# Kernel optimization log

Hardware: AMD Instinct MI355X
Metric: run time of the kernel (lower is better)

Reference implementation:

```python
import jax, jax.numpy as jnp
import numpy as np

B, L1, LQ, LA, H = 32, 512, 32, 32, 128  # dialog turns, doc len, q len, a len, hidden
NEG = -1e30  # finite stand-in for torch's -inf (avoids NaN for fully-masked row 0, which is dropped by zero_first anyway)


def setup_inputs() -> dict:
    key = jax.random.key(0)
    ks = jax.random.split(key, 6)
    return {
        "xd_emb": jax.random.normal(ks[0], (B, L1, H), jnp.float32),
        "xq_emb": jax.random.normal(ks[1], (B, LQ, H), jnp.float32),
        "xa_emb": jax.random.normal(ks[2], (B, LA, H), jnp.float32),
        "W": jax.random.normal(ks[3], (H, H), jnp.float32) / np.sqrt(H).astype(np.float32),
        "b": jnp.zeros((H,), jnp.float32),
        "recency_weight": jnp.full((1,), -0.5, jnp.float32),
        "xq_mask": jax.random.randint(ks[4], (B, LQ), 0, 2).astype(bool),
        "xa_mask": jax.random.randint(ks[5], (B, LA), 0, 2).astype(bool),
    }


def _forward(xd_emb, xq_emb, xa_emb, W, b, recency_weight, xq_mask, xa_mask):
    Bn = xq_emb.shape[0]
    M = xq_emb.shape[1] + xa_emb.shape[1]  # max_dialog_len (max_qa_len)
    dlg = jnp.concatenate([xq_emb, xa_emb], axis=1).reshape(Bn * M, -1)  # (B*M, h) flattened dialog
    pad_mask = jnp.concatenate([xq_mask, xa_mask], axis=1).reshape(-1)    # (B*M,)

    ts = jnp.arange(Bn)
    j_ts = jnp.arange(Bn * M) // M  # timestep of each flattened dialog token
    # triu(ones, k=0) repeated M times along cols: timestep i masks tokens of timesteps >= i
    causal = j_ts[None, :] >= ts[:, None]            # (B, B*M)
    y_mask = causal | pad_mask[None, :]              # (B, B*M), True = masked

    # Linear + ReLU projections; y_proj computed once (no explicit (B, B*M, h) tiling)
    x_proj = jax.nn.relu(xd_emb @ W.T + b)           # (B, L1, h)
    y_proj = jax.nn.relu(dlg @ W.T + b)              # (B*M, h)

    scores = jnp.einsum('bld,kd->blk', x_proj, y_proj)      # (B, L1, B*M)
    scores = jnp.where(y_mask[:, None, :], jnp.float32(NEG), scores)

    # toeplitz recency bias: |i - j_ts| * recency_weight, row 0 zeroed (zero_first)
    rw = recency_weight[0] * jnp.abs(ts[:, None] - j_ts[None, :]).astype(jnp.float32)
    rw = jnp.concatenate([jnp.zeros_like(rw[:1]), rw[1:]], axis=0)
    scores = scores + rw[:, None, :]

    alpha = jax.nn.softmax(scores, axis=-1)
    alpha = jnp.concatenate([jnp.zeros_like(alpha[:1]), alpha[1:]], axis=0)  # zero_first
    return jnp.einsum('blk,kd->bld', alpha, dlg)     # weighted sum over original (unprojected) dialog


def reference(xd_emb, xq_emb, xa_emb, W, b, recency_weight, xq_mask, xa_mask):
    return _forward(xd_emb, xq_emb, xa_emb, W, b, recency_weight, xq_mask, xa_mask)
```

## Files before the change

kernel.cpp:

```cpp
#include <hip/hip_runtime.h>
#include <stdint.h>

#define NEGV (-1e30f)

constexpr int L1_ = 512;
constexpr int H_  = 128;
constexpr int NK_ = 2048;

typedef __attribute__((ext_vector_type(8))) _Float16 f16x8;
typedef __attribute__((ext_vector_type(2))) __fp16   h16x2;
typedef __attribute__((ext_vector_type(4))) float    f32x4;

static __device__ __forceinline__ uint16_t f2h(float x) {
    union { _Float16 h; uint16_t u; } cv; cv.h = (_Float16)x; return cv.u;
}


__global__ __launch_bounds__(256) void preproc_kernel(
        const float* __restrict__ xq,
        const float* __restrict__ xa,
        const float* __restrict__ W,
        const float* __restrict__ bias,
        const uint8_t* __restrict__ qm,
        const uint8_t* __restrict__ am,
        uint8_t* __restrict__ Y2,
        uint8_t* __restrict__ V2,
        uint8_t* __restrict__ W2,
        float* __restrict__ badd) {
    int b = blockIdx.x;
    int tid = threadIdx.x;
    __shared__ __align__(16) float sbuf[64 * 128];

    if (b < 128) {
        int k0 = b * 16;
        f32x4* xr4 = (f32x4*)sbuf;
#pragma unroll
        for (int i = 0; i < 2; ++i) {
            int idx = tid + i * 256;
            int row = idx >> 5, d4 = idx & 31;
            int k = k0 + row;
            int b2 = k >> 6, r = k & 63;
            const float* src = (r < 32) ? (xq + (size_t)(b2 * 32 + r) * H_)
                                        : (xa + (size_t)(b2 * 32 + (r - 32)) * H_);
            xr4[idx] = *(const f32x4*)(src + d4 * 4);
        }
        __syncthreads();
        int c = tid & 127, rh = tid >> 7;
        float acc[8];
#pragma unroll
        for (int i = 0; i < 8; ++i) acc[i] = 0.0f;
        const f32x4* w4 = (const f32x4*)(W + (size_t)c * H_);
        for (int d4 = 0; d4 < 32; ++d4) {
            f32x4 wv = w4[d4];
#pragma unroll
            for (int i = 0; i < 8; ++i) {
                f32x4 x = xr4[(rh * 8 + i) * 32 + d4];
                acc[i] += wv[0]*x[0] + wv[1]*x[1] + wv[2]*x[2] + wv[3]*x[3];
            }
        }
        float bc = bias[c];
        float* res = sbuf + 2048;
#pragma unroll
        for (int i = 0; i < 8; ++i)
            res[(rh * 8 + i) * H_ + c] = fmaxf(acc[i] + bc, 0.0f);
        __syncthreads();
        int ks = tid >> 6, l = tid & 63, n16 = l & 15, g = l >> 4;
        uint16_t hbuf[8];
#pragma unroll
        for (int j = 0; j < 8; ++j)
            hbuf[j] = f2h(res[n16 * H_ + ks * 32 + g * 8 + j]);
        uint8_t* dst = Y2 + (((size_t)b * 4 + ks) << 10) + l * 16;
        *(uint64_t*)dst       = ((const uint64_t*)hbuf)[0];
        *(uint64_t*)(dst + 8) = ((const uint64_t*)hbuf)[1];
    } else if (b < 160) {
        int kt = b - 128;
        f32x4* ld4 = (f32x4*)sbuf;
#pragma unroll
        for (int i = 0; i < 8; ++i) {
            int idx = tid + i * 256;
            int row = idx >> 5, d4 = idx & 31;
            const float* src = (row < 32) ? (xq + (size_t)(kt * 32 + row) * H_)
                                          : (xa + (size_t)(kt * 32 + row - 32) * H_);
            ld4[idx] = *(const f32x4*)(src + d4 * 4);
        }
        __syncthreads();
#pragma unroll
        for (int i = 0; i < 4; ++i) {
            int id = tid + i * 256;
            int cT = id >> 7, ks = (id >> 6) & 1, l = id & 63;
            int n16 = l & 15, g = l >> 4;
            uint16_t hbuf[8];
#pragma unroll
            for (int j = 0; j < 8; ++j)
                hbuf[j] = f2h(sbuf[(ks * 32 + g * 8 + j) * H_ + cT * 16 + n16]);
            uint8_t* dst = V2 + (((size_t)kt * 16 + cT * 2 + ks) << 10) + l * 16;
            *(uint64_t*)dst       = ((const uint64_t*)hbuf)[0];
            *(uint64_t*)(dst + 8) = ((const uint64_t*)hbuf)[1];
        }
    } else if (b == 160) {
        int* flags = (int*)sbuf;
        if (tid == 0) { flags[0] = 0; flags[1] = 0; }
        __syncthreads();
        uint32_t v = ((const uint32_t*)qm)[tid] | ((const uint32_t*)am)[tid];
        if (v & 0xFFu)        atomicOr(&flags[0], 1);
        if (v & 0xFFFFFF00u)  atomicOr(&flags[1], 1);
        __syncthreads();
        int f0 = flags[0], f1 = flags[1];
        int mode = (f0 && !f1) ? 0 : ((!f0 && f1) ? 1 : 2);
        for (int k = tid; k < NK_; k += 256) {
            int b2 = k >> 6, r = k & 63;
            int idx = b2 * 32 + (r < 32 ? r : r - 32);
            const uint8_t* src = (r < 32) ? qm : am;
            int p;
            if (mode == 0)      p = (((const int*)src)[idx] != 0);
            else if (mode == 1) p = (((const float*)src)[idx] != 0.0f);
            else                p = (src[idx] != 0);
            badd[k] = p ? NEGV : 0.0f;
        }
    } else {
        for (int h = 0; h < 2; ++h) {
            f32x4* s4 = (f32x4*)sbuf;
#pragma unroll
            for (int i = 0; i < 8; ++i) {
                int idx = tid + i * 256;
                s4[idx] = *(const f32x4*)(W + (size_t)h * 64 * H_ + idx * 4);
            }
            __syncthreads();
#pragma unroll
            for (int i = 0; i < 4; ++i) {
                int id = tid + i * 256;
                int ct = id >> 8, ks = (id >> 6) & 3, l = id & 63;
                int n16 = l & 15, g = l >> 4;
                uint16_t hb[8];
#pragma unroll
                for (int j = 0; j < 8; ++j)
                    hb[j] = f2h(sbuf[(ct * 16 + n16) * H_ + ks * 32 + g * 8 + j]);
                uint8_t* dst = W2 + (((size_t)((h * 4 + ct) * 4 + ks)) << 10) + l * 16;
                *(uint64_t*)dst       = ((const uint64_t*)hb)[0];
                *(uint64_t*)(dst + 8) = ((const uint64_t*)hb)[1];
            }
            __syncthreads();
        }
    }
}

__global__ __launch_bounds__(512, 2) void attn_kernel(
        const float*   __restrict__ xd,
        const uint8_t* __restrict__ W2,
        const float*   __restrict__ bias,
        const uint8_t* __restrict__ Y2,
        const uint8_t* __restrict__ V2,
        const float*   __restrict__ badd,
        const float*   __restrict__ rw,
        float* __restrict__ out) {
    int bid = blockIdx.x;
    int t, lt;
    if (bid < 256) { int p = bid >> 4; t = (p < 15) ? 31 - p : 16; lt = bid & 15; }
    else           { int b2 = bid - 256; int p = b2 >> 4; t = (p < 15) ? p + 1 : 0; lt = b2 & 15; }
    int l0 = lt << 5;
    int tid = threadIdx.x;

    __shared__ __align__(16) float smem[16384];
    __shared__ float stats_m[8][32];
    __shared__ float stats_l[8][32];

    if (t == 0) {
        f32x4 z = {0.f, 0.f, 0.f, 0.f};
        f32x4* o4 = (f32x4*)(out + (size_t)l0 * H_);
        for (int i = tid; i < 32 * H_ / 4; i += 512) o4[i] = z;
        return;
    }

    int w = tid >> 6, lane = tid & 63, n16 = lane & 15, g = lane >> 4;
    int prow0 = n16, prow1 = 16 + n16;
    int swzP = (n16 & 7) << 4;

    uint16_t* xbuf  = (uint16_t*)((char*)smem + 32768);
    uint16_t* xpbuf = (uint16_t*)((char*)smem + 40960);
    {
        const float* xsrc = xd + (size_t)(t * L1_ + l0) * H_;
#pragma unroll
        for (int i = 0; i < 2; ++i) {
            int idx = tid + i * 512;
            int row = idx >> 5, c4 = idx & 31;
            f32x4 v = *(const f32x4*)(xsrc + idx * 4);
            uint16_t hb[4] = { f2h(v[0]), f2h(v[1]), f2h(v[2]), f2h(v[3]) };
            *(uint64_t*)((char*)xbuf + row * 256 + ((c4 * 8) ^ ((row & 7) << 4)))
                = *(const uint64_t*)hb;
        }
    }
    __syncthreads();
    {
        f16x8 af[2][4];
#pragma unroll
        for (int rT = 0; rT < 2; ++rT) {
            int row = rT * 16 + n16, swz = (row & 7) << 4;
#pragma unroll
            for (int ks = 0; ks < 4; ++ks)
                af[rT][ks] = *(const f16x8*)((char*)xbuf + row * 256 + ((ks * 64 + g * 16) ^ swz));
        }
        f32x4 z4 = {0.f, 0.f, 0.f, 0.f};
        f32x4 d0 = z4, d1 = z4;
#pragma unroll
        for (int ks = 0; ks < 4; ++ks) {
            f16x8 wf = *(const f16x8*)(W2 + (((size_t)w * 4 + ks) << 10) + lane * 16);
            d0 = __builtin_amdgcn_mfma_f32_16x16x32_f16(af[0][ks], wf, d0, 0, 0, 0);
            d1 = __builtin_amdgcn_mfma_f32_16x16x32_f16(af[1][ks], wf, d1, 0, 0, 0);
        }
        float bb = bias[w * 16 + n16];
#pragma unroll
        for (int rT = 0; rT < 2; ++rT) {
            const f32x4& d = rT ? d1 : d0;
#pragma unroll
            for (int q = 0; q < 4; ++q) {
                int row = rT * 16 + g * 4 + q, swz = (row & 7) << 4;
                *(uint16_t*)((char*)xpbuf + row * 256 + (((w * 16 + n16) * 2) ^ swz))
                    = f2h(fmaxf(d[q] + bb, 0.0f));
            }
        }
    }
    __syncthreads();
    f16x8 xf[2][4];
#pragma unroll
    for (int rT = 0; rT < 2; ++rT) {
        int row = rT * 16 + n16, swz = (row & 7) << 4;
#pragma unroll
        for (int ks = 0; ks < 4; ++ks)
            xf[rT][ks] = *(const f16x8*)((char*)xpbuf + row * 256 + ((ks * 64 + g * 16) ^ swz));
    }

    f32x4 zero4 = {0.f, 0.f, 0.f, 0.f};
    f32x4 acc[2][8];
#pragma unroll
    for (int a = 0; a < 2; ++a)
#pragma unroll
        for (int c = 0; c < 8; ++c) acc[a][c] = zero4;

    float m_r[2] = {-INFINITY, -INFINITY};
    float l_r[2] = {0.0f, 0.0f};
    float rww = rw[0];

    char* Pw = (char*)smem + w * 4096;

    for (int kt = w; kt < t; kt += 8) {
        const uint8_t* ybase = Y2 + ((size_t)kt << 14) + lane * 16;
        const uint8_t* vbase = V2 + ((size_t)kt << 14) + lane * 16;

        f16x8 yf[4][4];
#pragma unroll
        for (int kkT = 0; kkT < 4; ++kkT)
#pragma unroll
            for (int ks = 0; ks < 4; ++ks)
                yf[kkT][ks] = *(const f16x8*)(ybase + ((kkT * 4 + ks) << 10));
        f16x8 vbA[4][2];
#pragma unroll
        for (int cT = 0; cT < 4; ++cT) {
            vbA[cT][0] = *(const f16x8*)(vbase + ((cT * 2) << 10));
            vbA[cT][1] = *(const f16x8*)(vbase + ((cT * 2 + 1) << 10));
        }
        f32x4 ba4[4];
#pragma unroll
        for (int kkT = 0; kkT < 4; ++kkT)
            ba4[kkT] = *(const f32x4*)(badd + kt * 64 + kkT * 16 + g * 4);

        f32x4 ss[4][2];
#pragma unroll
        for (int kkT = 0; kkT < 4; ++kkT) { ss[kkT][0] = zero4; ss[kkT][1] = zero4; }
        __builtin_amdgcn_s_setprio(1);
#pragma unroll
        for (int ks = 0; ks < 4; ++ks)
#pragma unroll
            for (int kkT = 0; kkT < 4; ++kkT) {
                ss[kkT][0] = __builtin_amdgcn_mfma_f32_16x16x32_f16(yf[kkT][ks], xf[0][ks], ss[kkT][0], 0, 0, 0);
                ss[kkT][1] = __builtin_amdgcn_mfma_f32_16x16x32_f16(yf[kkT][ks], xf[1][ks], ss[kkT][1], 0, 0, 0);
            }
        __builtin_amdgcn_s_setprio(0);

        f16x8 vbB[4][2];
#pragma unroll
        for (int cT = 0; cT < 4; ++cT) {
            vbB[cT][0] = *(const f16x8*)(vbase + (((cT + 4) * 2) << 10));
            vbB[cT][1] = *(const f16x8*)(vbase + (((cT + 4) * 2 + 1) << 10));
        }

        float biasK = rww * (float)(t - kt);
#pragma unroll
        for (int kkT = 0; kkT < 4; ++kkT) {
            f32x4 ba = ba4[kkT] + biasK;
            ss[kkT][0] += ba;
            ss[kkT][1] += ba;
        }

        float sc[2];
#pragma unroll
        for (int rT = 0; rT < 2; ++rT) {
            f32x4 mx4 = ss[0][rT];
#pragma unroll
            for (int kkT = 1; kkT < 4; ++kkT) {
                mx4[0] = fmaxf(mx4[0], ss[kkT][rT][0]);
                mx4[1] = fmaxf(mx4[1], ss[kkT][rT][1]);
                mx4[2] = fmaxf(mx4[2], ss[kkT][rT][2]);
                mx4[3] = fmaxf(mx4[3], ss[kkT][rT][3]);
            }
            float mx = fmaxf(fmaxf(mx4[0], mx4[1]), fmaxf(mx4[2], mx4[3]));
            mx = fmaxf(mx, __shfl_xor(mx, 16));
            mx = fmaxf(mx, __shfl_xor(mx, 32));
            float mn = fmaxf(m_r[rT], mx);
            sc[rT] = __expf(m_r[rT] - mn);
            m_r[rT] = mn;
        }

#pragma unroll
        for (int rT = 0; rT < 2; ++rT) {
            int r = rT ? prow1 : prow0;
            float mn = m_r[rT];
            float ps = 0.0f;
#pragma unroll
            for (int kkT = 0; kkT < 4; ++kkT) {
                f32x4 p;
#pragma unroll
                for (int q = 0; q < 4; ++q) p[q] = __expf(ss[kkT][rT][q] - mn);
                ps += (p[0] + p[1]) + (p[2] + p[3]);
                union { h16x2 h2[2]; uint64_t u64; } pk;
                pk.h2[0] = __builtin_amdgcn_cvt_pkrtz(p[0], p[1]);
                pk.h2[1] = __builtin_amdgcn_cvt_pkrtz(p[2], p[3]);
                *(uint64_t*)(Pw + r * 128 + ((kkT * 32 + g * 8) ^ swzP)) = pk.u64;
            }
            ps += __shfl_xor(ps, 16);
            ps += __shfl_xor(ps, 32);
            l_r[rT] = l_r[rT] * sc[rT] + ps;
        }

        asm volatile("s_waitcnt lgkmcnt(0)" ::: "memory");

        if (!__all((sc[0] == 1.0f) && (sc[1] == 1.0f))) {
#pragma unroll
            for (int rT = 0; rT < 2; ++rT) {
                f32x4 s4;
#pragma unroll
                for (int q = 0; q < 4; ++q) s4[q] = __shfl(sc[rT], (g << 2) + q);
#pragma unroll
                for (int cT = 0; cT < 8; ++cT) acc[rT][cT] *= s4;
            }
        }

        f16x8 pa[2][2];
#pragma unroll
        for (int rT = 0; rT < 2; ++rT) {
            int r = rT ? prow1 : prow0;
#pragma unroll
            for (int ks = 0; ks < 2; ++ks)
                pa[rT][ks] = *(const f16x8*)(Pw + r * 128 + ((ks * 64 + g * 16) ^ swzP));
        }
        __builtin_amdgcn_s_setprio(1);
#pragma unroll
        for (int cT = 0; cT < 4; ++cT)
#pragma unroll
            for (int rT = 0; rT < 2; ++rT) {
                acc[rT][cT] = __builtin_amdgcn_mfma_f32_16x16x32_f16(pa[rT][0], vbA[cT][0], acc[rT][cT], 0, 0, 0);
                acc[rT][cT] = __builtin_amdgcn_mfma_f32_16x16x32_f16(pa[rT][1], vbA[cT][1], acc[rT][cT], 0, 0, 0);
            }
#pragma unroll
        for (int cT = 0; cT < 4; ++cT)
#pragma unroll
            for (int rT = 0; rT < 2; ++rT) {
                acc[rT][cT + 4] = __builtin_amdgcn_mfma_f32_16x16x32_f16(pa[rT][0], vbB[cT][0], acc[rT][cT + 4], 0, 0, 0);
                acc[rT][cT + 4] = __builtin_amdgcn_mfma_f32_16x16x32_f16(pa[rT][1], vbB[cT][1], acc[rT][cT + 4], 0, 0, 0);
            }
        __builtin_amdgcn_s_setprio(0);
    }

    if (g == 0) {
        stats_m[w][n16]      = m_r[0];
        stats_m[w][16 + n16] = m_r[1];
        stats_l[w][n16]      = l_r[0];
        stats_l[w][16 + n16] = l_r[1];
    }
    __syncthreads();

    float fac[2][4];
#pragma unroll
    for (int rT = 0; rT < 2; ++rT)
#pragma unroll
        for (int q = 0; q < 4; ++q) {
            int r = rT * 16 + (g << 2) + q;
            float mf = stats_m[0][r];
#pragma unroll
            for (int wv = 1; wv < 8; ++wv) mf = fmaxf(mf, stats_m[wv][r]);
            float lf = 0.0f;
#pragma unroll
            for (int wv = 0; wv < 8; ++wv) lf += stats_l[wv][r] * __expf(stats_m[wv][r] - mf);
            fac[rT][q] = __expf(stats_m[w][r] - mf) / lf;
        }

    size_t obase = (size_t)(t * L1_ + l0) * H_;
    for (int rT = 0; rT < 2; ++rT) {
        float* Ob = smem + w * 2048;
#pragma unroll
        for (int cT = 0; cT < 8; ++cT)
#pragma unroll
            for (int q = 0; q < 4; ++q)
                Ob[(cT * 4 + q) * 64 + lane] = acc[rT][cT][q] * fac[rT][q];
        __syncthreads();
#pragma unroll
        for (int s = 0; s < 4; ++s) {
            int slot = w * 4 + s;
            float v = 0.0f;
#pragma unroll
            for (int wv = 0; wv < 8; ++wv) v += smem[wv * 2048 + slot * 64 + lane];
            int cT = slot >> 2, q = slot & 3;
            out[obase + (size_t)(rT * 16 + (g << 2) + q) * H_ + cT * 16 + n16] = v;
        }
        __syncthreads();
    }
}

extern "C" void kernel_launch(void* const* d_in, const int* in_sizes, int n_in,
                              void* d_out, int out_size, void* d_ws, size_t ws_size,
                              hipStream_t stream) {
    const float*   xd   = (const float*)d_in[0];
    const float*   xq   = (const float*)d_in[1];
    const float*   xa   = (const float*)d_in[2];
    const float*   W    = (const float*)d_in[3];
    const float*   bias = (const float*)d_in[4];
    const float*   rw   = (const float*)d_in[5];
    const uint8_t* qm   = (const uint8_t*)d_in[6];
    const uint8_t* am   = (const uint8_t*)d_in[7];
    float* out = (float*)d_out;

    char* ws = (char*)d_ws;
    float*   badd = (float*)ws;
    uint8_t* Y2   = (uint8_t*)(ws + 8192);
    uint8_t* V2   = (uint8_t*)(ws + 8192 + 524288);
    uint8_t* W2   = (uint8_t*)(ws + 8192 + 2 * 524288);

    preproc_kernel<<<162, 256, 0, stream>>>(xq, xa, W, bias, qm, am,
                                            Y2, V2, W2, badd);
    attn_kernel<<<512, 512, 0, stream>>>(xd, W2, bias, Y2, V2, badd, rw, out);
}
```

Baseline: 44.74 us.

## Restructure attention kernel with LDS double-buffered K/V tiles and 64-row blocks

The attention kernel now processes 64 query rows per block, using 256 blocks instead of 512. Four row groups each take two key-timestep halves. Y and V tiles for each pair of timesteps are staged into LDS with global_load_lds, double-buffered so the next pair loads while the current one computes. Previously every wave read Y and V straight from global memory. The two half-softmax partials are merged at the end through LDS. The trade-offs are one block per CU with about 144KB of LDS, a __syncthreads per iteration, and the removal of the old load-balancing block order across timesteps.

```diff
diff --git a/kernel.cpp b/kernel.cpp
--- a/kernel.cpp
+++ b/kernel.cpp
@@ -13,6 +13,12 @@
 
 static __device__ __forceinline__ uint16_t f2h(float x) {
     union { _Float16 h; uint16_t u; } cv; cv.h = (_Float16)x; return cv.u;
+}
+
+static __device__ __forceinline__ void gload16(const void* g, void* l) {
+    __builtin_amdgcn_global_load_lds(
+        (const __attribute__((address_space(1))) uint32_t*)g,
+        (__attribute__((address_space(3))) uint32_t*)l, 16, 0, 0);
 }
 
 
@@ -144,7 +150,7 @@
     }
 }
 
-__global__ __launch_bounds__(512, 2) void attn_kernel(
+__global__ __launch_bounds__(512, 1) void attn_kernel(
         const float*   __restrict__ xd,
         const uint8_t* __restrict__ W2,
         const float*   __restrict__ bias,
@@ -154,264 +160,241 @@
         const float*   __restrict__ rw,
         float* __restrict__ out) {
     int bid = blockIdx.x;
-    int t, lt;
-    if (bid < 256) { int p = bid >> 4; t = (p < 15) ? 31 - p : 16; lt = bid & 15; }
-    else           { int b2 = bid - 256; int p = b2 >> 4; t = (p < 15) ? p + 1 : 0; lt = b2 & 15; }
-    int l0 = lt << 5;
+    int t  = bid >> 3;
+    int l0 = (bid & 7) << 6;
     int tid = threadIdx.x;
 
-    __shared__ __align__(16) float smem[16384];
-    __shared__ float stats_m[8][32];
-    __shared__ float stats_l[8][32];
+    __shared__ __align__(16) char LDSA[147456];
+    __shared__ float stats_m[8][16];
+    __shared__ float stats_l[8][16];
 
     if (t == 0) {
         f32x4 z = {0.f, 0.f, 0.f, 0.f};
         f32x4* o4 = (f32x4*)(out + (size_t)l0 * H_);
-        for (int i = tid; i < 32 * H_ / 4; i += 512) o4[i] = z;
+        for (int i = tid; i < 64 * H_ / 4; i += 512) o4[i] = z;
         return;
     }
 
     int w = tid >> 6, lane = tid & 63, n16 = lane & 15, g = lane >> 4;
-    int prow0 = n16, prow1 = 16 + n16;
-    int swzP = (n16 & 7) << 4;
-
-    uint16_t* xbuf  = (uint16_t*)((char*)smem + 32768);
-    uint16_t* xpbuf = (uint16_t*)((char*)smem + 40960);
+    int rg = w & 3, kh = w >> 2;
+    int swz = (n16 & 7) << 4;
+
+    {
+        char* ld = LDSA;
+        gload16(Y2 + tid * 16,        ld + tid * 16);
+        gload16(Y2 + tid * 16 + 8192, ld + tid * 16 + 8192);
+        gload16(V2 + tid * 16,         ld + 16384 + tid * 16);
+        gload16(V2 + tid * 16 + 8192,  ld + 24576 + tid * 16);
+        if (1 < t) {
+            const uint8_t* gy = Y2 + (1 << 14);
+            const uint8_t* gv = V2 + (1 << 14);
+            char* ld2 = LDSA + 32768;
+            gload16(gy + tid * 16,        ld2 + tid * 16);
+            gload16(gy + tid * 16 + 8192, ld2 + tid * 16 + 8192);
+            gload16(gv + tid * 16,         ld2 + 16384 + tid * 16);
+            gload16(gv + tid * 16 + 8192,  ld2 + 24576 + tid * 16);
+        }
+    }
+
+    char* xbuf  = LDSA + 65536;
+    char* xpbuf = LDSA + 131072;
     {
         const float* xsrc = xd + (size_t)(t * L1_ + l0) * H_;
 #pragma unroll
-        for (int i = 0; i < 2; ++i) {
+        for (int i = 0; i < 4; ++i) {
             int idx = tid + i * 512;
             int row = idx >> 5, c4 = idx & 31;
             f32x4 v = *(const f32x4*)(xsrc + idx * 4);
             uint16_t hb[4] = { f2h(v[0]), f2h(v[1]), f2h(v[2]), f2h(v[3]) };
-            *(uint64_t*)((char*)xbuf + row * 256 + ((c4 * 8) ^ ((row & 7) << 4)))
-                = *(const uint64_t*)hb;
+            *(uint64_t*)(xbuf + row * 256 + ((c4 * 8) ^ ((row & 7) << 4))) = *(const uint64_t*)hb;
         }
     }
     __syncthreads();
     {
-        f16x8 af[2][4];
-#pragma unroll
-        for (int rT = 0; rT < 2; ++rT) {
-            int row = rT * 16 + n16, swz = (row & 7) << 4;
-#pragma unroll
-            for (int ks = 0; ks < 4; ++ks)
-                af[rT][ks] = *(const f16x8*)((char*)xbuf + row * 256 + ((ks * 64 + g * 16) ^ swz));
-        }
+        f16x8 af[4];
+        int arow = rg * 16 + n16;
+#pragma unroll
+        for (int ks = 0; ks < 4; ++ks)
+            af[ks] = *(const f16x8*)(xbuf + arow * 256 + ((ks * 64 + g * 16) ^ swz));
         f32x4 z4 = {0.f, 0.f, 0.f, 0.f};
-        f32x4 d0 = z4, d1 = z4;
-#pragma unroll
-        for (int ks = 0; ks < 4; ++ks) {
-            f16x8 wf = *(const f16x8*)(W2 + (((size_t)w * 4 + ks) << 10) + lane * 16);
-            d0 = __builtin_amdgcn_mfma_f32_16x16x32_f16(af[0][ks], wf, d0, 0, 0, 0);
-            d1 = __builtin_amdgcn_mfma_f32_16x16x32_f16(af[1][ks], wf, d1, 0, 0, 0);
-        }
-        float bb = bias[w * 16 + n16];
-#pragma unroll
-        for (int rT = 0; rT < 2; ++rT) {
-            const f32x4& d = rT ? d1 : d0;
+        f32x4 d[4] = {z4, z4, z4, z4};
+#pragma unroll
+        for (int c = 0; c < 4; ++c)
+#pragma unroll
+            for (int ks = 0; ks < 4; ++ks) {
+                f16x8 wf = *(const f16x8*)(W2 + (((size_t)(kh * 4 + c) * 4 + ks) << 10) + lane * 16);
+                d[c] = __builtin_amdgcn_mfma_f32_16x16x32_f16(af[ks], wf, d[c], 0, 0, 0);
+            }
+#pragma unroll
+        for (int c = 0; c < 4; ++c) {
+            int col = (kh * 4 + c) * 16 + n16;
+            float bb = bias[col];
 #pragma unroll
             for (int q = 0; q < 4; ++q) {
-                int row = rT * 16 + g * 4 + q, swz = (row & 7) << 4;
-                *(uint16_t*)((char*)xpbuf + row * 256 + (((w * 16 + n16) * 2) ^ swz))
-                    = f2h(fmaxf(d[q] + bb, 0.0f));
+                int row2 = rg * 16 + g * 4 + q;
+                *(uint16_t*)(xpbuf + row2 * 256 + ((col * 2) ^ ((row2 & 7) << 4)))
+                    = f2h(fmaxf(d[c][q] + bb, 0.0f));
             }
         }
     }
     __syncthreads();
-    f16x8 xf[2][4];
-#pragma unroll
-    for (int rT = 0; rT < 2; ++rT) {
-        int row = rT * 16 + n16, swz = (row & 7) << 4;
+    f16x8 xf[4];
+    {
+        int arow = rg * 16 + n16;
 #pragma unroll
         for (int ks = 0; ks < 4; ++ks)
-            xf[rT][ks] = *(const f16x8*)((char*)xpbuf + row * 256 + ((ks * 64 + g * 16) ^ swz));
-    }
+            xf[ks] = *(const f16x8*)(xpbuf + arow * 256 + ((ks * 64 + g * 16) ^ swz));
+    }
+    __syncthreads();
 
     f32x4 zero4 = {0.f, 0.f, 0.f, 0.f};
-    f32x4 acc[2][8];
-#pragma unroll
-    for (int a = 0; a < 2; ++a)
-#pragma unroll
-        for (int c = 0; c < 8; ++c) acc[a][c] = zero4;
-
-    float m_r[2] = {-INFINITY, -INFINITY};
-    float l_r[2] = {0.0f, 0.0f};
+    f32x4 acc[8];
+#pragma unroll
+    for (int c = 0; c < 8; ++c) acc[c] = zero4;
+    float m_r = -INFINITY, l_r = 0.0f;
     float rww = rw[0];
-
-    char* Pw = (char*)smem + w * 4096;
-
-    for (int kt = w; kt < t; kt += 8) {
-        const uint8_t* ybase = Y2 + ((size_t)kt << 14) + lane * 16;
-        const uint8_t* vbase = V2 + ((size_t)kt << 14) + lane * 16;
-
-        f16x8 yf[4][4];
-#pragma unroll
-        for (int kkT = 0; kkT < 4; ++kkT)
-#pragma unroll
-            for (int ks = 0; ks < 4; ++ks)
-                yf[kkT][ks] = *(const f16x8*)(ybase + ((kkT * 4 + ks) << 10));
-        f16x8 vbA[4][2];
-#pragma unroll
-        for (int cT = 0; cT < 4; ++cT) {
-            vbA[cT][0] = *(const f16x8*)(vbase + ((cT * 2) << 10));
-            vbA[cT][1] = *(const f16x8*)(vbase + ((cT * 2 + 1) << 10));
-        }
-        f32x4 ba4[4];
-#pragma unroll
-        for (int kkT = 0; kkT < 4; ++kkT)
-            ba4[kkT] = *(const f32x4*)(badd + kt * 64 + kkT * 16 + g * 4);
-
-        f32x4 ss[4][2];
-#pragma unroll
-        for (int kkT = 0; kkT < 4; ++kkT) { ss[kkT][0] = zero4; ss[kkT][1] = zero4; }
-        __builtin_amdgcn_s_setprio(1);
-#pragma unroll
-        for (int ks = 0; ks < 4; ++ks)
+    char* Pw = LDSA + 131072 + w * 2048;
+    int nR = (t + 1) >> 1;
+
+    for (int i = 0; i < nR; ++i) {
+        int cur = i & 1;
+        if (i + 1 < nR) {
+            int kt0 = 2 * (i + 1);
+            char* ld = LDSA + (cur ? 0 : 65536);
+            const uint8_t* gy = Y2 + ((size_t)kt0 << 14);
+            const uint8_t* gv = V2 + ((size_t)kt0 << 14);
+            gload16(gy + tid * 16,        ld + tid * 16);
+            gload16(gy + tid * 16 + 8192, ld + tid * 16 + 8192);
+            gload16(gv + tid * 16,         ld + 16384 + tid * 16);
+            gload16(gv + tid * 16 + 8192,  ld + 24576 + tid * 16);
+            if (kt0 + 1 < t) {
+                gy += (1 << 14); gv += (1 << 14);
+                char* ld2 = ld + 32768;
+                gload16(gy + tid * 16,        ld2 + tid * 16);
+                gload16(gy + tid * 16 + 8192, ld2 + tid * 16 + 8192);
+                gload16(gv + tid * 16,         ld2 + 16384 + tid * 16);
+                gload16(gv + tid * 16 + 8192,  ld2 + 24576 + tid * 16);
+            }
+        }
+
+        int kt = 2 * i + kh;
+        if (kt < t) {
+            const char* Yb = LDSA + (cur ? 65536 : 0) + kh * 32768;
+            const char* Vb = Yb + 16384;
+
+            f32x4 ss[4];
+#pragma unroll
+            for (int kkT = 0; kkT < 4; ++kkT) ss[kkT] = zero4;
+            __builtin_amdgcn_s_setprio(1);
+#pragma unroll
+            for (int ks = 0; ks < 4; ++ks) {
+                f16x8 yf[4];
+#pragma unroll
+                for (int kkT = 0; kkT < 4; ++kkT)
+                    yf[kkT] = *(const f16x8*)(Yb + ((kkT * 4 + ks) << 10) + lane * 16);
+#pragma unroll
+                for (int kkT = 0; kkT < 4; ++kkT)
+                    ss[kkT] = __builtin_amdgcn_mfma_f32_16x16x32_f16(yf[kkT], xf[ks], ss[kkT], 0, 0, 0);
+            }
+            __builtin_amdgcn_s_setprio(0);
+
+            float biasK = rww * (float)(t - kt);
 #pragma unroll
             for (int kkT = 0; kkT < 4; ++kkT) {
-                ss[kkT][0] = __builtin_amdgcn_mfma_f32_16x16x32_f16(yf[kkT][ks], xf[0][ks], ss[kkT][0], 0, 0, 0);
-                ss[kkT][1] = __builtin_amdgcn_mfma_f32_16x16x32_f16(yf[kkT][ks], xf[1][ks], ss[kkT][1], 0, 0, 0);
-            }
-        __builtin_amdgcn_s_setprio(0);
-
-        f16x8 vbB[4][2];
-#pragma unroll
-        for (int cT = 0; cT < 4; ++cT) {
-            vbB[cT][0] = *(const f16x8*)(vbase + (((cT + 4) * 2) << 10));
-            vbB[cT][1] = *(const f16x8*)(vbase + (((cT + 4) * 2 + 1) << 10));
-        }
-
-        float biasK = rww * (float)(t - kt);
-#pragma unroll
-        for (int kkT = 0; kkT < 4; ++kkT) {
-            f32x4 ba = ba4[kkT] + biasK;
-            ss[kkT][0] += ba;
-            ss[kkT][1] += ba;
-        }
-
-        float sc[2];
-#pragma unroll
-        for (int rT = 0; rT < 2; ++rT) {
-            f32x4 mx4 = ss[0][rT];
+                f32x4 ba = *(const f32x4*)(badd + kt * 64 + kkT * 16 + g * 4);
+                ss[kkT] += (ba + biasK);
+            }
+
+            f32x4 mx4 = ss[0];
 #pragma unroll
             for (int kkT = 1; kkT < 4; ++kkT) {
-                mx4[0] = fmaxf(mx4[0], ss[kkT][rT][0]);
-                mx4[1] = fmaxf(mx4[1], ss[kkT][rT][1]);
-                mx4[2] = fmaxf(mx4[2], ss[kkT][rT][2]);
-                mx4[3] = fmaxf(mx4[3], ss[kkT][rT][3]);
+                mx4[0] = fmaxf(mx4[0], ss[kkT][0]);
+                mx4[1] = fmaxf(mx4[1], ss[kkT][1]);
+                mx4[2] = fmaxf(mx4[2], ss[kkT][2]);
+                mx4[3] = fmaxf(mx4[3], ss[kkT][3]);
             }
             float mx = fmaxf(fmaxf(mx4[0], mx4[1]), fmaxf(mx4[2], mx4[3]));
             mx = fmaxf(mx, __shfl_xor(mx, 16));
             mx = fmaxf(mx, __shfl_xor(mx, 32));
-            float mn = fmaxf(m_r[rT], mx);
-            sc[rT] = __expf(m_r[rT] - mn);
-            m_r[rT] = mn;
-        }
-
-#pragma unroll
-        for (int rT = 0; rT < 2; ++rT) {
-            int r = rT ? prow1 : prow0;
-            float mn = m_r[rT];
+            float mn = fmaxf(m_r, mx);
+            float sc = __expf(m_r - mn);
+            m_r = mn;
+
             float ps = 0.0f;
 #pragma unroll
             for (int kkT = 0; kkT < 4; ++kkT) {
                 f32x4 p;
 #pragma unroll
-                for (int q = 0; q < 4; ++q) p[q] = __expf(ss[kkT][rT][q] - mn);
+                for (int q = 0; q < 4; ++q) p[q] = __expf(ss[kkT][q] - mn);
                 ps += (p[0] + p[1]) + (p[2] + p[3]);
                 union { h16x2 h2[2]; uint64_t u64; } pk;
                 pk.h2[0] = __builtin_amdgcn_cvt_pkrtz(p[0], p[1]);
                 pk.h2[1] = __builtin_amdgcn_cvt_pkrtz(p[2], p[3]);
-                *(uint64_t*)(Pw + r * 128 + ((kkT * 32 + g * 8) ^ swzP)) = pk.u64;
+                *(uint64_t*)(Pw + n16 * 128 + ((kkT * 32 + g * 8) ^ swz)) = pk.u64;
             }
             ps += __shfl_xor(ps, 16);
             ps += __shfl_xor(ps, 32);
-            l_r[rT] = l_r[rT] * sc[rT] + ps;
-        }
-
-        asm volatile("s_waitcnt lgkmcnt(0)" ::: "memory");
-
-        if (!__all((sc[0] == 1.0f) && (sc[1] == 1.0f))) {
-#pragma unroll
-            for (int rT = 0; rT < 2; ++rT) {
+            l_r = l_r * sc + ps;
+
+            asm volatile("s_waitcnt lgkmcnt(0)" ::: "memory");
+
+            if (!__all(sc == 1.0f)) {
                 f32x4 s4;
 #pragma unroll
-                for (int q = 0; q < 4; ++q) s4[q] = __shfl(sc[rT], (g << 2) + q);
-#pragma unroll
-                for (int cT = 0; cT < 8; ++cT) acc[rT][cT] *= s4;
-            }
-        }
-
-        f16x8 pa[2][2];
-#pragma unroll
-        for (int rT = 0; rT < 2; ++rT) {
-            int r = rT ? prow1 : prow0;
-#pragma unroll
-            for (int ks = 0; ks < 2; ++ks)
-                pa[rT][ks] = *(const f16x8*)(Pw + r * 128 + ((ks * 64 + g * 16) ^ swzP));
-        }
-        __builtin_amdgcn_s_setprio(1);
-#pragma unroll
-        for (int cT = 0; cT < 4; ++cT)
-#pragma unroll
-            for (int rT = 0; rT < 2; ++rT) {
-                acc[rT][cT] = __builtin_amdgcn_mfma_f32_16x16x32_f16(pa[rT][0], vbA[cT][0], acc[rT][cT], 0, 0, 0);
-                acc[rT][cT] = __builtin_amdgcn_mfma_f32_16x16x32_f16(pa[rT][1], vbA[cT][1], acc[rT][cT], 0, 0, 0);
-            }
-#pragma unroll
-        for (int cT = 0; cT < 4; ++cT)
-#pragma unroll
-            for (int rT = 0; rT < 2; ++rT) {
-                acc[rT][cT + 4] = __builtin_amdgcn_mfma_f32_16x16x32_f16(pa[rT][0], vbB[cT][0], acc[rT][cT + 4], 0, 0, 0);
-                acc[rT][cT + 4] = __builtin_amdgcn_mfma_f32_16x16x32_f16(pa[rT][1], vbB[cT][1], acc[rT][cT + 4], 0, 0, 0);
-            }
-        __builtin_amdgcn_s_setprio(0);
-    }
-
-    if (g == 0) {
-        stats_m[w][n16]      = m_r[0];
-        stats_m[w][16 + n16] = m_r[1];
-        stats_l[w][n16]      = l_r[0];
-        stats_l[w][16 + n16] = l_r[1];
-    }
+                for (int q = 0; q < 4; ++q) s4[q] = __shfl(sc, (g << 2) + q);
+#pragma unroll
+                for (int c = 0; c < 8; ++c) acc[c] *= s4;
+            }
+
+            f16x8 pa0 = *(const f16x8*)(Pw + n16 * 128 + ((g * 16) ^ swz));
+            f16x8 pa1 = *(const f16x8*)(Pw + n16 * 128 + ((64 + g * 16) ^ swz));
+            __builtin_amdgcn_s_setprio(1);
+#pragma unroll
+            for (int cT = 0; cT < 8; ++cT) {
+                f16x8 vb0 = *(const f16x8*)(Vb + ((cT * 2) << 10) + lane * 16);
+                f16x8 vb1 = *(const f16x8*)(Vb + ((cT * 2 + 1) << 10) + lane * 16);
+                acc[cT] = __builtin_amdgcn_mfma_f32_16x16x32_f16(pa0, vb0, acc[cT], 0, 0, 0);
+                acc[cT] = __builtin_amdgcn_mfma_f32_16x16x32_f16(pa1, vb1, acc[cT], 0, 0, 0);
+            }
+            __builtin_amdgcn_s_setprio(0);
+        }
+        __syncthreads();
+    }
+
+    if (g == 0) { stats_m[w][n16] = m_r; stats_l[w][n16] = l_r; }
     __syncthreads();
 
-    float fac[2][4];
-#pragma unroll
-    for (int rT = 0; rT < 2; ++rT)
-#pragma unroll
-        for (int q = 0; q < 4; ++q) {
-            int r = rT * 16 + (g << 2) + q;
-            float mf = stats_m[0][r];
-#pragma unroll
-            for (int wv = 1; wv < 8; ++wv) mf = fmaxf(mf, stats_m[wv][r]);
-            float lf = 0.0f;
-#pragma unroll
-            for (int wv = 0; wv < 8; ++wv) lf += stats_l[wv][r] * __expf(stats_m[wv][r] - mf);
-            fac[rT][q] = __expf(stats_m[w][r] - mf) / lf;
-        }
-
-    size_t obase = (size_t)(t * L1_ + l0) * H_;
-    for (int rT = 0; rT < 2; ++rT) {
-        float* Ob = smem + w * 2048;
+    int pw = w ^ 4;
+    float fac[4];
+#pragma unroll
+    for (int q = 0; q < 4; ++q) {
+        int r = (g << 2) + q;
+        float ma = stats_m[w][r],  mb = stats_m[pw][r];
+        float la = stats_l[w][r],  lb = stats_l[pw][r];
+        float mf = fmaxf(ma, mb);
+        float lf = la * __expf(ma - mf) + lb * __expf(mb - mf);
+        fac[q] = __expf(ma - mf) / lf;
+    }
+
+    float* Ob = (float*)LDSA;
+    if (kh == 1) {
 #pragma unroll
         for (int cT = 0; cT < 8; ++cT)
 #pragma unroll
             for (int q = 0; q < 4; ++q)
-                Ob[(cT * 4 + q) * 64 + lane] = acc[rT][cT][q] * fac[rT][q];
-        __syncthreads();
-#pragma unroll
-        for (int s = 0; s < 4; ++s) {
-            int slot = w * 4 + s;
-            float v = 0.0f;
-#pragma unroll
-            for (int wv = 0; wv < 8; ++wv) v += smem[wv * 2048 + slot * 64 + lane];
-            int cT = slot >> 2, q = slot & 3;
-            out[obase + (size_t)(rT * 16 + (g << 2) + q) * H_ + cT * 16 + n16] = v;
-        }
-        __syncthreads();
+                Ob[(rg * 16 + g * 4 + q) * 128 + cT * 16 + n16] = acc[cT][q] * fac[q];
+    }
+    __syncthreads();
+    if (kh == 0) {
+        size_t ob = (size_t)(t * L1_ + l0 + rg * 16) * H_;
+#pragma unroll
+        for (int cT = 0; cT < 8; ++cT)
+#pragma unroll
+            for (int q = 0; q < 4; ++q) {
+                float v = acc[cT][q] * fac[q]
+                        + Ob[(rg * 16 + g * 4 + q) * 128 + cT * 16 + n16];
+                out[ob + (size_t)(g * 4 + q) * H_ + cT * 16 + n16] = v;
+            }
     }
 }
 
@@ -436,5 +419,5 @@
 
     preproc_kernel<<<162, 256, 0, stream>>>(xq, xa, W, bias, qm, am,
                                             Y2, V2, W2, badd);
-    attn_kernel<<<512, 512, 0, stream>>>(xd, W2, bias, Y2, V2, badd, rw, out);
+    attn_kernel<<<256, 512, 0, stream>>>(xd, W2, bias, Y2, V2, badd, rw, out);
 }
```

Result: slower. 49.55 us (+10.7%).
